# Optimization experiments

Measured on AMD Instinct MI355X. Metric: run time of the kernel, lower is better.

Reference implementation:

```python
import jax, jax.numpy as jnp
import numpy as np

B, N, M, ZD, YD, XD = 4, 512, 512, 128, 2, 1


def setup_inputs() -> dict:
    key = jax.random.key(0)
    k_t, k_z, k_x, k_w = jax.random.split(key, 4)
    return {
        "t": jax.random.normal(k_t, (B, N, XD), dtype=jnp.float32),
        "z": jax.random.normal(k_z, (B, N, ZD), dtype=jnp.float32),
        "x": jax.random.normal(k_x, (B, M, XD), dtype=jnp.float32),
        "sigma": jnp.zeros((ZD,), dtype=jnp.float32),  # log(length_scale=1) = 0
        "W": jax.random.normal(k_w, (YD, ZD), dtype=jnp.float32) * (1.0 / np.sqrt(ZD)),
        "b": jnp.zeros((YD,), dtype=jnp.float32),
    }


def reference(t, z, x, sigma, W, b):
    # diff: (b, n, m) -- sum over x_dim as in the torch code, then channelized
    diff = (x[:, None, :, :] - t[:, :, None, :]).sum(-1)
    scale = jnp.exp(sigma)  # (c,)
    # kernel: (b, n, m, c) RBF weights per channel
    kernel = jnp.exp(-0.5 * (diff[..., None] / scale) ** 2)
    # z-weighted reduction over grid points n -> (b, m, c)
    y = jnp.einsum("bnc,bnmc->bmc", z, kernel)
    # final linear: (b, m, y_dim)
    return y @ W.T + b
```

## Files before the change

### kernel.cpp

```cpp
#include <hip/hip_runtime.h>
#include <math.h>

#define B_  4
#define N_  512
#define M_  512
#define ZD_ 128
#define YD_ 2

#define LOG2E_HALF 0.72134752044f

#define WS_A2   0
#define WS_FLAG 128
#define WS_ZW   192

__global__ __launch_bounds__(256)
void prep_kernel(const float* __restrict__ z,
                 const float* __restrict__ sigma,
                 const float* __restrict__ W,
                 float* __restrict__ ws)
{
    __shared__ float Wl[YD_ * ZD_];
    __shared__ int oks;

    const int b   = blockIdx.x;
    const int tid = threadIdx.x;

    if (tid == 0) oks = 1;
    if (tid < (YD_ * ZD_) / 4)
        ((float4*)Wl)[tid] = ((const float4*)W)[tid];
    __syncthreads();

    for (int n = tid; n < N_; n += 256) {
        const float4* zr = (const float4*)(z + ((size_t)b * N_ + n) * ZD_);
        float s0 = 0.f, s1 = 0.f;
        #pragma unroll 8
        for (int k = 0; k < ZD_ / 4; ++k) {
            const float4 zv = zr[k];
            const float4 w0 = ((const float4*)Wl)[k];
            const float4 w1 = ((const float4*)Wl)[ZD_ / 4 + k];
            s0 = fmaf(zv.x, w0.x, fmaf(zv.y, w0.y, fmaf(zv.z, w0.z, fmaf(zv.w, w0.w, s0))));
            s1 = fmaf(zv.x, w1.x, fmaf(zv.y, w1.y, fmaf(zv.z, w1.z, fmaf(zv.w, w1.w, s1))));
        }
        ws[WS_ZW + b * (N_ * YD_) + n * YD_ + 0] = s0;
        ws[WS_ZW + b * (N_ * YD_) + n * YD_ + 1] = s1;
    }

    if (b == 0) {
        if (tid < ZD_) {
            const float sc  = __expf(sigma[tid]);
            const float a2  = -LOG2E_HALF / (sc * sc);
            const float sc0 = __expf(sigma[0]);
            const float a20 = -LOG2E_HALF / (sc0 * sc0);
            ws[WS_A2 + tid] = a2;
            if (a2 != a20) oks = 0;
        }
        __syncthreads();
        if (tid == 0) ws[WS_FLAG] = oks ? 1.0f : 0.0f;
    }
}

__global__ __launch_bounds__(256)
void decode_kernel(const float* __restrict__ t,
                   const float* __restrict__ z,
                   const float* __restrict__ x,
                   const float* __restrict__ W,
                   const float* __restrict__ bias,
                   const float* __restrict__ ws,
                   float* __restrict__ out)
{
    __shared__ float ts[N_];
    __shared__ float zwl[N_][YD_];
    __shared__ float pr[4][64][YD_];
    __shared__ float Wl[YD_ * ZD_];

    const int b   = blockIdx.y;
    const int m0  = blockIdx.x * 64;
    const int tid = threadIdx.x;
    const int w   = tid >> 6;
    const int l   = tid & 63;

    for (int i = tid; i < N_; i += 256)
        ts[i] = t[(size_t)b * N_ + i];
    for (int i = tid; i < N_ * YD_; i += 256)
        ((float*)zwl)[i] = ws[WS_ZW + b * (N_ * YD_) + i];
    if (tid < (YD_ * ZD_) / 4)
        ((float4*)Wl)[tid] = ((const float4*)W)[tid];
    __syncthreads();

    const int   m  = m0 + l;
    const float xm = x[(size_t)b * M_ + m];
    const float uf = ws[WS_FLAG];

    float s0 = 0.f, s1 = 0.f;
    if (uf != 0.f) {
        const float a2 = ws[WS_A2];
        #pragma unroll 8
        for (int i = 0; i < N_ / 4; ++i) {
            const int   n = w * (N_ / 4) + i;
            const float d = xm - ts[n];
            const float e = __builtin_amdgcn_exp2f(a2 * d * d);
            s0 = fmaf(zwl[n][0], e, s0);
            s1 = fmaf(zwl[n][1], e, s1);
        }
    } else {
        for (int i = 0; i < N_ / 4; ++i) {
            const int   n  = w * (N_ / 4) + i;
            const float d  = xm - ts[n];
            const float d2 = d * d;
            const float* zr = z + ((size_t)b * N_ + n) * ZD_;
            for (int c = 0; c < ZD_; ++c) {
                const float e = __builtin_amdgcn_exp2f(ws[WS_A2 + c] * d2);
                const float p = zr[c] * e;
                s0 = fmaf(Wl[c],        p, s0);
                s1 = fmaf(Wl[ZD_ + c],  p, s1);
            }
        }
    }

    pr[w][l][0] = s0;
    pr[w][l][1] = s1;
    __syncthreads();

    if (tid < 64) {
        float r0 = bias[0], r1 = bias[1];
        #pragma unroll
        for (int g = 0; g < 4; ++g) {
            r0 += pr[g][tid][0];
            r1 += pr[g][tid][1];
        }
        *(float2*)(out + ((size_t)b * M_ + m0 + tid) * YD_) = make_float2(r0, r1);
    }
}

extern "C" void kernel_launch(void* const* d_in, const int* in_sizes, int n_in,
                              void* d_out, int out_size, void* d_ws, size_t ws_size,
                              hipStream_t stream) {
    const float* t     = (const float*)d_in[0];
    const float* z     = (const float*)d_in[1];
    const float* x     = (const float*)d_in[2];
    const float* sigma = (const float*)d_in[3];
    const float* W     = (const float*)d_in[4];
    const float* bias  = (const float*)d_in[5];
    float* out = (float*)d_out;
    float* ws  = (float*)d_ws;

    prep_kernel<<<dim3(B_), dim3(256), 0, stream>>>(z, sigma, W, ws);
    decode_kernel<<<dim3(M_ / 64, B_), dim3(256), 0, stream>>>(t, z, x, W, bias, ws, out);
}
```

Measured before the change: 77.47 us.

## Fuse prep and decode kernels, recomputing z·W projection per block in shared memory

Merges the prep kernel (z projected onto W, sigma scale check) into the decode kernel, so each block computes its batch's z·W projection and uniform-sigma flag directly into shared memory. This removes a second kernel launch and the workspace round trip through global memory. In exchange, every block in a batch redundantly reads the full z slice for that batch (8x redundant z traffic) and does the projection work, which lengthens each block's prologue. The fallback path now recomputes per-channel scales inline.

```diff
diff --git a/kernel.cpp b/kernel.cpp
--- a/kernel.cpp
+++ b/kernel.cpp
@@ -9,28 +9,45 @@
 
 #define LOG2E_HALF 0.72134752044f
 
-#define WS_A2   0
-#define WS_FLAG 128
-#define WS_ZW   192
+__global__ __launch_bounds__(256)
+void decoder_fused(const float* __restrict__ t,
+                   const float* __restrict__ z,
+                   const float* __restrict__ x,
+                   const float* __restrict__ sigma,
+                   const float* __restrict__ W,
+                   const float* __restrict__ bias,
+                   float* __restrict__ out)
+{
+    __shared__ float ts[N_];
+    __shared__ float zw0[N_];
+    __shared__ float zw1[N_];
+    __shared__ float Wl[YD_ * ZD_];
+    __shared__ float pr[4][64][YD_];
+    __shared__ float a2s;
+    __shared__ int   oks;
 
-__global__ __launch_bounds__(256)
-void prep_kernel(const float* __restrict__ z,
-                 const float* __restrict__ sigma,
-                 const float* __restrict__ W,
-                 float* __restrict__ ws)
-{
-    __shared__ float Wl[YD_ * ZD_];
-    __shared__ int oks;
-
-    const int b   = blockIdx.x;
+    const int b   = blockIdx.y;
+    const int m0  = blockIdx.x * 64;
     const int tid = threadIdx.x;
+    const int w   = tid >> 6;
+    const int l   = tid & 63;
 
     if (tid == 0) oks = 1;
     if (tid < (YD_ * ZD_) / 4)
         ((float4*)Wl)[tid] = ((const float4*)W)[tid];
     __syncthreads();
 
+    if (tid < ZD_) {
+        const float sc  = __expf(sigma[tid]);
+        const float a2  = -LOG2E_HALF / (sc * sc);
+        const float sc0 = __expf(sigma[0]);
+        const float a20 = -LOG2E_HALF / (sc0 * sc0);
+        if (a2 != a20) oks = 0;
+        if (tid == 0) a2s = a20;
+    }
+
     for (int n = tid; n < N_; n += 256) {
+        ts[n] = t[(size_t)b * N_ + n];
         const float4* zr = (const float4*)(z + ((size_t)b * N_ + n) * ZD_);
         float s0 = 0.f, s1 = 0.f;
         #pragma unroll 8
@@ -41,66 +58,24 @@
             s0 = fmaf(zv.x, w0.x, fmaf(zv.y, w0.y, fmaf(zv.z, w0.z, fmaf(zv.w, w0.w, s0))));
             s1 = fmaf(zv.x, w1.x, fmaf(zv.y, w1.y, fmaf(zv.z, w1.z, fmaf(zv.w, w1.w, s1))));
         }
-        ws[WS_ZW + b * (N_ * YD_) + n * YD_ + 0] = s0;
-        ws[WS_ZW + b * (N_ * YD_) + n * YD_ + 1] = s1;
+        zw0[n] = s0;
+        zw1[n] = s1;
     }
-
-    if (b == 0) {
-        if (tid < ZD_) {
-            const float sc  = __expf(sigma[tid]);
-            const float a2  = -LOG2E_HALF / (sc * sc);
-            const float sc0 = __expf(sigma[0]);
-            const float a20 = -LOG2E_HALF / (sc0 * sc0);
-            ws[WS_A2 + tid] = a2;
-            if (a2 != a20) oks = 0;
-        }
-        __syncthreads();
-        if (tid == 0) ws[WS_FLAG] = oks ? 1.0f : 0.0f;
-    }
-}
-
-__global__ __launch_bounds__(256)
-void decode_kernel(const float* __restrict__ t,
-                   const float* __restrict__ z,
-                   const float* __restrict__ x,
-                   const float* __restrict__ W,
-                   const float* __restrict__ bias,
-                   const float* __restrict__ ws,
-                   float* __restrict__ out)
-{
-    __shared__ float ts[N_];
-    __shared__ float zwl[N_][YD_];
-    __shared__ float pr[4][64][YD_];
-    __shared__ float Wl[YD_ * ZD_];
-
-    const int b   = blockIdx.y;
-    const int m0  = blockIdx.x * 64;
-    const int tid = threadIdx.x;
-    const int w   = tid >> 6;
-    const int l   = tid & 63;
-
-    for (int i = tid; i < N_; i += 256)
-        ts[i] = t[(size_t)b * N_ + i];
-    for (int i = tid; i < N_ * YD_; i += 256)
-        ((float*)zwl)[i] = ws[WS_ZW + b * (N_ * YD_) + i];
-    if (tid < (YD_ * ZD_) / 4)
-        ((float4*)Wl)[tid] = ((const float4*)W)[tid];
     __syncthreads();
 
     const int   m  = m0 + l;
     const float xm = x[(size_t)b * M_ + m];
-    const float uf = ws[WS_FLAG];
 
     float s0 = 0.f, s1 = 0.f;
-    if (uf != 0.f) {
-        const float a2 = ws[WS_A2];
+    if (oks) {
+        const float a2 = a2s;
         #pragma unroll 8
         for (int i = 0; i < N_ / 4; ++i) {
             const int   n = w * (N_ / 4) + i;
             const float d = xm - ts[n];
             const float e = __builtin_amdgcn_exp2f(a2 * d * d);
-            s0 = fmaf(zwl[n][0], e, s0);
-            s1 = fmaf(zwl[n][1], e, s1);
+            s0 = fmaf(zw0[n], e, s0);
+            s1 = fmaf(zw1[n], e, s1);
         }
     } else {
         for (int i = 0; i < N_ / 4; ++i) {
@@ -109,10 +84,12 @@
             const float d2 = d * d;
             const float* zr = z + ((size_t)b * N_ + n) * ZD_;
             for (int c = 0; c < ZD_; ++c) {
-                const float e = __builtin_amdgcn_exp2f(ws[WS_A2 + c] * d2);
-                const float p = zr[c] * e;
-                s0 = fmaf(Wl[c],        p, s0);
-                s1 = fmaf(Wl[ZD_ + c],  p, s1);
+                const float sc = __expf(sigma[c]);
+                const float ac = -LOG2E_HALF / (sc * sc);
+                const float e  = __builtin_amdgcn_exp2f(ac * d2);
+                const float p  = zr[c] * e;
+                s0 = fmaf(Wl[c],       p, s0);
+                s1 = fmaf(Wl[ZD_ + c], p, s1);
             }
         }
     }
@@ -142,8 +119,7 @@
     const float* W     = (const float*)d_in[4];
     const float* bias  = (const float*)d_in[5];
     float* out = (float*)d_out;
-    float* ws  = (float*)d_ws;
 
-    prep_kernel<<<dim3(B_), dim3(256), 0, stream>>>(z, sigma, W, ws);
-    decode_kernel<<<dim3(M_ / 64, B_), dim3(256), 0, stream>>>(t, z, x, W, bias, ws, out);
+    decoder_fused<<<dim3(M_ / 64, B_), dim3(256), 0, stream>>>(
+        t, z, x, sigma, W, bias, out);
 }
```

New measurement: 75.40 us. 2.7% less time.
